# Performance work log

Measured on AMD Instinct MI355X. Metric: run time of the kernel, lower is better.

Reference implementation:

```python
import jax, jax.numpy as jnp
import numpy as np

N_USERS = 100000
N_ITEMS = 50000
N = N_USERS + N_ITEMS  # graph nodes
E = 2_400_000
B = 16384
EMB = 64
HID = 128
LN_EPS = 1e-5


def _gcn(x, W, b, src, dst):
    # PyG GCNConv (eval): sym-normalized aggregation with self-loops.
    xw = x @ W                                      # [N, out]
    deg = jnp.ones((N,), x.dtype).at[dst].add(1.0)  # in-degree + self-loop
    dinv = jax.lax.rsqrt(deg)
    norm = dinv[src] * dinv[dst]                    # [E]
    msg = xw[src] * norm[:, None]                   # [E, out] gather
    out = jax.ops.segment_sum(msg, dst, num_segments=N)
    out = out + xw * (dinv * dinv)[:, None]         # self-loop term (norm_ii = 1/deg_i)
    return out + b


def _ln(h, g, b):
    mu = jnp.mean(h, axis=-1, keepdims=True)
    var = jnp.mean(jnp.square(h - mu), axis=-1, keepdims=True)
    return (h - mu) * jax.lax.rsqrt(var + LN_EPS) * g + b


def setup_inputs() -> dict:
    key = jax.random.key(0)
    ks = jax.random.split(key, 20)
    f32 = jnp.float32
    def lin(k, fi, fo):
        return jax.random.normal(k, (fi, fo), f32) * (1.0 / np.sqrt(fi))
    inp = {
        "x": jax.random.normal(ks[0], (N, EMB), f32),
        "src": jax.random.randint(ks[1], (E,), 0, N, jnp.int32),
        "dst": jax.random.randint(ks[2], (E,), 0, N, jnp.int32),
        "user_indices": jax.random.randint(ks[3], (B,), 1, N_USERS + 1, jnp.int32),
        "item_indices": jax.random.randint(ks[4], (B,), 1, N_ITEMS + 1, jnp.int32),
        # GCNConv weights
        "W1": lin(ks[5], EMB, HID), "b1": jnp.zeros((HID,), f32),
        "W2": lin(ks[6], HID, EMB), "b2": jnp.zeros((EMB,), f32),
        # MLP head: Linear(128,128)-LN-ReLU-Linear(128,64)-LN-ReLU-Linear(64,1)
        "fcW1": lin(ks[7], 2 * EMB, HID), "fcb1": jnp.zeros((HID,), f32),
        "g1": jnp.ones((HID,), f32), "be1": jnp.zeros((HID,), f32),
        "fcW2": lin(ks[8], HID, HID // 2), "fcb2": jnp.zeros((HID // 2,), f32),
        "g2": jnp.ones((HID // 2,), f32), "be2": jnp.zeros((HID // 2,), f32),
        "fcW3": lin(ks[9], HID // 2, 1), "fcb3": jnp.zeros((1,), f32),
    }
    return inp


def reference(x, src, dst, user_indices, item_indices,
              W1, b1, W2, b2,
              fcW1, fcb1, g1, be1, fcW2, fcb2, g2, be2, fcW3, fcb3):
    # graph path (edge_index and x provided); dropout inactive in eval mode
    h = jax.nn.relu(_gcn(x, W1, b1, src, dst))
    h = _gcn(h, W2, b2, src, dst)                   # [N, EMB]
    user_emb = h[:N_USERS][user_indices - 1]        # [B, EMB]
    item_emb = h[N_USERS:][item_indices - 1]        # [B, EMB]
    c = jnp.concatenate([user_emb, item_emb], axis=1)  # [B, 2*EMB]
    z = jax.nn.relu(_ln(c @ fcW1 + fcb1, g1, be1))
    z = jax.nn.relu(_ln(z @ fcW2 + fcb2, g2, be2))
    z = z @ fcW3 + fcb3                             # [B, 1]
    return jax.nn.sigmoid(z).squeeze()
```

## Files before the change

### kernel.cpp

```cpp
#include <hip/hip_runtime.h>
#include <hip/hip_bf16.h>
#include <math.h>

#define N_USERS_C 100000
#define BK_SHIFT 9
#define BK_NODES 512
#define CPAD 16

typedef __bf16 bf8_t __attribute__((ext_vector_type(8)));
typedef float f32x4 __attribute__((ext_vector_type(4)));

__device__ __forceinline__ unsigned int pack_bf16(float a, float b) {
    __hip_bfloat16 ha = __float2bfloat16(a), hb = __float2bfloat16(b);
    return ((unsigned int)(*(unsigned short*)&hb) << 16) | (unsigned int)(*(unsigned short*)&ha);
}
__device__ __forceinline__ unsigned short bf16_1(float a) {
    __hip_bfloat16 ha = __float2bfloat16(a);
    return *(unsigned short*)&ha;
}
__device__ __forceinline__ float bf_lo(unsigned int u) { return __uint_as_float(u << 16); }
__device__ __forceinline__ float bf_hi(unsigned int u) { return __uint_as_float(u & 0xffff0000u); }

__global__ __launch_bounds__(512) void k_pre(const int* __restrict__ dst, int* __restrict__ chist,
                                             const float* __restrict__ x, unsigned int* __restrict__ xb,
                                             const float* __restrict__ W1, const float* __restrict__ W2,
                                             unsigned int* __restrict__ w1p, unsigned int* __restrict__ w2p,
                                             int E, int nbk, int EB2, int n2, int XB) {
    __shared__ int lcnt[BK_NODES];
    const int bid = blockIdx.x;
    const int t = threadIdx.x;
    if (bid < EB2) {
        if (t < nbk) lcnt[t] = 0;
        __syncthreads();
        int e0 = bid * 4096;
        #pragma unroll
        for (int j = 0; j < 8; ++j) {
            int e = e0 + j * 512 + t;
            if (e < E) atomicAdd(&lcnt[dst[e] >> BK_SHIFT], 1);
        }
        __syncthreads();
        if (t < nbk && lcnt[t]) atomicAdd(&chist[t * CPAD], lcnt[t]);
    } else if (bid < EB2 + XB) {
        int base = (bid - EB2) * 2048;
        #pragma unroll
        for (int j = 0; j < 4; ++j) {
            int i = base + j * 512 + t;
            if (i < n2) {
                float2 v = ((const float2*)x)[i];
                xb[i] = pack_bf16(v.x, v.y);
            }
        }
    } else if (bid == EB2 + XB) {
        #pragma unroll
        for (int j = 0; j < 8; ++j) {
            int i = j * 512 + t;
            int kp = i >> 7, n = i & 127;
            w1p[n * 32 + kp] = pack_bf16(W1[(size_t)(2 * kp) * 128 + n],
                                         W1[(size_t)(2 * kp + 1) * 128 + n]);
        }
    } else {
        #pragma unroll
        for (int j = 0; j < 8; ++j) {
            int i = j * 512 + t;
            int kp = i >> 6, n = i & 63;
            w2p[n * 64 + kp] = pack_bf16(W2[(size_t)(2 * kp) * 64 + n],
                                         W2[(size_t)(2 * kp + 1) * 64 + n]);
        }
    }
}

__global__ __launch_bounds__(512) void k_bin(const int* __restrict__ src,
                                             const int* __restrict__ dst,
                                             const int* __restrict__ chist,
                                             int* __restrict__ bcursor0,
                                             int* __restrict__ pairBuf, int E, int nbk) {
    __shared__ int lcnt[BK_NODES];
    __shared__ int lofs[BK_NODES];
    __shared__ int delta[BK_NODES];
    __shared__ int waveSum[8];
    __shared__ int sPack[4096];
    __shared__ unsigned short sBkt[4096];
    const int t = threadIdx.x;
    const int lane = t & 63;
    const int w = t >> 6;
    const int e0 = blockIdx.x * 4096;
    if (t < nbk) lcnt[t] = 0;
    __syncthreads();

    int mySrc[8], myB[8], myDl[8];
    #pragma unroll
    for (int j = 0; j < 8; ++j) {
        int e = e0 + j * 512 + t;
        if (e < E) {
            int sv = src[e], dv = dst[e];
            mySrc[j] = sv; myB[j] = dv >> BK_SHIFT; myDl[j] = dv & (BK_NODES - 1);
            atomicAdd(&lcnt[myB[j]], 1);
        } else myB[j] = -1;
    }
    __syncthreads();

    int v = (t < nbk) ? lcnt[t] : 0;
    int inc = v;
    #pragma unroll
    for (int off = 1; off < 64; off <<= 1) {
        int n = __shfl_up(inc, off);
        if (lane >= off) inc += n;
    }
    if (lane == 63) waveSum[w] = inc;
    int cv = (t < nbk) ? chist[t * CPAD] : 0;
    int cinc = cv;
    #pragma unroll
    for (int off = 1; off < 64; off <<= 1) {
        int n = __shfl_up(cinc, off);
        if (lane >= off) cinc += n;
    }
    __shared__ int cWaveSum[8];
    if (lane == 63) cWaveSum[w] = cinc;
    __syncthreads();
    int wp = 0, cwp = 0;
    #pragma unroll
    for (int i = 0; i < 8; ++i) {
        wp += (i < w) ? waveSum[i] : 0;
        cwp += (i < w) ? cWaveSum[i] : 0;
    }
    int ex = wp + inc - v;
    int cbase = cwp + cinc - cv;
    if (t < nbk) {
        lofs[t] = ex;
        int gb = cbase + ((v > 0) ? atomicAdd(&bcursor0[t * CPAD], v) : 0);
        delta[t] = gb - ex;
    }
    __syncthreads();

    #pragma unroll
    for (int j = 0; j < 8; ++j) {
        if (myB[j] >= 0) {
            int p = atomicAdd(&lofs[myB[j]], 1);
            sPack[p] = mySrc[j] | (myDl[j] << 18);
            sBkt[p] = (unsigned short)myB[j];
        }
    }
    __syncthreads();
    int total = (E - e0 < 4096) ? (E - e0) : 4096;
    for (int i = t; i < total; i += 512)
        pairBuf[delta[sBkt[i]] + i] = sPack[i];
}

__global__ __launch_bounds__(512) void k_bscatter(const int* __restrict__ pairBuf,
                                                  const int* __restrict__ chist,
                                                  int* __restrict__ rowstart,
                                                  float* __restrict__ dinv,
                                                  int* __restrict__ csr,
                                                  unsigned int* __restrict__ xb,
                                                  int N, int E, int nbk) {
    const int b = blockIdx.x;
    const int n0 = b << BK_SHIFT;
    int nn = N - n0; if (nn > BK_NODES) nn = BK_NODES;
    __shared__ int hist[BK_NODES];
    __shared__ int curs[BK_NODES];
    __shared__ float sdv[BK_NODES];
    __shared__ int waveSum[8];
    __shared__ int sE0, sE1;
    const int t = threadIdx.x;
    const int lane = t & 63;
    const int w = t >> 6;

    {
        int cv = (t < nbk) ? chist[t * CPAD] : 0;
        int cinc = cv;
        #pragma unroll
        for (int off = 1; off < 64; off <<= 1) {
            int n = __shfl_up(cinc, off);
            if (lane >= off) cinc += n;
        }
        if (lane == 63) waveSum[w] = cinc;
        if (t < nn) hist[t] = 0;
        __syncthreads();
        int cwp = 0;
        #pragma unroll
        for (int i = 0; i < 8; ++i) cwp += (i < w) ? waveSum[i] : 0;
        if (t == b) { sE0 = cwp + cinc - cv; sE1 = cwp + cinc; }
    }
    __syncthreads();
    const int e0 = sE0, e1 = sE1;

    {
        int e = e0 + t;
        for (; e + 1536 < e1; e += 2048) {
            int p0 = pairBuf[e], p1 = pairBuf[e + 512];
            int p2 = pairBuf[e + 1024], p3 = pairBuf[e + 1536];
            atomicAdd(&hist[p0 >> 18], 1);
            atomicAdd(&hist[p1 >> 18], 1);
            atomicAdd(&hist[p2 >> 18], 1);
            atomicAdd(&hist[p3 >> 18], 1);
        }
        for (; e < e1; e += 512)
            atomicAdd(&hist[pairBuf[e] >> 18], 1);
    }
    __syncthreads();

    int v = (t < nn) ? hist[t] : 0;
    int inc = v;
    #pragma unroll
    for (int off = 1; off < 64; off <<= 1) {
        int n = __shfl_up(inc, off);
        if (lane >= off) inc += n;
    }
    if (lane == 63) waveSum[w] = inc;
    __syncthreads();
    int wp = 0;
    #pragma unroll
    for (int i = 0; i < 8; ++i) wp += (i < w) ? waveSum[i] : 0;
    int ex = wp + inc - v;
    if (t < nn) {
        int r = e0 + ex;
        rowstart[n0 + t] = r;
        curs[t] = r;
        float dv = rsqrtf((float)(v + 1));
        dinv[n0 + t] = dv;
        sdv[t] = dv;
    }
    if (b == gridDim.x - 1 && t == 0) rowstart[N] = E;
    __syncthreads();
    {
        int e = e0 + t;
        for (; e + 1536 < e1; e += 2048) {
            int p0 = pairBuf[e], p1 = pairBuf[e + 512];
            int p2 = pairBuf[e + 1024], p3 = pairBuf[e + 1536];
            int q0 = atomicAdd(&curs[p0 >> 18], 1); csr[q0] = p0 & 0x3FFFF;
            int q1 = atomicAdd(&curs[p1 >> 18], 1); csr[q1] = p1 & 0x3FFFF;
            int q2 = atomicAdd(&curs[p2 >> 18], 1); csr[q2] = p2 & 0x3FFFF;
            int q3 = atomicAdd(&curs[p3 >> 18], 1); csr[q3] = p3 & 0x3FFFF;
        }
        for (; e < e1; e += 512) {
            int pk = pairBuf[e];
            int pos = atomicAdd(&curs[pk >> 18], 1);
            csr[pos] = pk & 0x3FFFF;
        }
    }
    {
        uint4* xb4 = (uint4*)(xb + (size_t)n0 * 32);
        int tot = nn * 8;
        for (int j = t; j < tot; j += 1024) {
            int j2 = j + 512;
            uint4 u = xb4[j];
            uint4 u2;
            bool two = (j2 < tot);
            if (two) u2 = xb4[j2];
            float dv = sdv[j >> 3];
            u.x = pack_bf16(dv * bf_lo(u.x), dv * bf_hi(u.x));
            u.y = pack_bf16(dv * bf_lo(u.y), dv * bf_hi(u.y));
            u.z = pack_bf16(dv * bf_lo(u.z), dv * bf_hi(u.z));
            u.w = pack_bf16(dv * bf_lo(u.w), dv * bf_hi(u.w));
            xb4[j] = u;
            if (two) {
                float dv2 = sdv[j2 >> 3];
                u2.x = pack_bf16(dv2 * bf_lo(u2.x), dv2 * bf_hi(u2.x));
                u2.y = pack_bf16(dv2 * bf_lo(u2.y), dv2 * bf_hi(u2.y));
                u2.z = pack_bf16(dv2 * bf_lo(u2.z), dv2 * bf_hi(u2.z));
                u2.w = pack_bf16(dv2 * bf_lo(u2.w), dv2 * bf_hi(u2.w));
                xb4[j2] = u2;
            }
        }
    }
}

__global__ __launch_bounds__(256) void k_gather1(const int* __restrict__ rowstart,
                                                 const int* __restrict__ csr,
                                                 const float* __restrict__ dinv,
                                                 const uint4* __restrict__ xb4,
                                                 unsigned int* __restrict__ outb, int N) {
    const int l = threadIdx.x & 63;
    const int w = threadIdx.x >> 6;
    const int half = l >> 5;
    const int h = l & 31;
    const int sub = h >> 3;
    const int c = h & 7;
    const int hb = half * 32;
    const int node = blockIdx.x * 8 + w * 2 + half;
    if (node >= N) return;
    const int rs = rowstart[node];
    const int re = rowstart[node + 1];
    uint4 us = xb4[(size_t)node * 8 + c];
    float dd = dinv[node];

    float acc[8] = {0.f, 0.f, 0.f, 0.f, 0.f, 0.f, 0.f, 0.f};
    for (int base = rs; base < re; base += 32) {
        int idx = base + h;
        int sE = (idx < re) ? csr[idx] : 0;
        int cnt = re - base; if (cnt > 32) cnt = 32;
        int groups = (cnt + 3) >> 2;
        uint4 u0, u1, u2, u3;
        {
            int sk;
            if (0 < groups) { sk = __shfl(sE, hb + 0 + sub);  u0 = xb4[(size_t)sk * 8 + c]; }
            if (1 < groups) { sk = __shfl(sE, hb + 4 + sub);  u1 = xb4[(size_t)sk * 8 + c]; }
            if (2 < groups) { sk = __shfl(sE, hb + 8 + sub);  u2 = xb4[(size_t)sk * 8 + c]; }
            if (3 < groups) { sk = __shfl(sE, hb + 12 + sub); u3 = xb4[(size_t)sk * 8 + c]; }
        }
        #define ACC8(uu) { acc[0] += bf_lo(uu.x); acc[1] += bf_hi(uu.x); \
                           acc[2] += bf_lo(uu.y); acc[3] += bf_hi(uu.y); \
                           acc[4] += bf_lo(uu.z); acc[5] += bf_hi(uu.z); \
                           acc[6] += bf_lo(uu.w); acc[7] += bf_hi(uu.w); }
        for (int g = 0; g < groups; g += 4) {
            uint4 c0 = u0, c1 = u1, c2 = u2, c3 = u3;
            {
                int sk;
                if (g + 4 < groups) { sk = __shfl(sE, hb + (g + 4) * 4 + sub); u0 = xb4[(size_t)sk * 8 + c]; }
                if (g + 5 < groups) { sk = __shfl(sE, hb + (g + 5) * 4 + sub); u1 = xb4[(size_t)sk * 8 + c]; }
                if (g + 6 < groups) { sk = __shfl(sE, hb + (g + 6) * 4 + sub); u2 = xb4[(size_t)sk * 8 + c]; }
                if (g + 7 < groups) { sk = __shfl(sE, hb + (g + 7) * 4 + sub); u3 = xb4[(size_t)sk * 8 + c]; }
            }
            if ((g + 0) * 4 + sub < cnt) ACC8(c0);
            if ((g + 1) * 4 + sub < cnt) ACC8(c1);
            if ((g + 2) * 4 + sub < cnt) ACC8(c2);
            if ((g + 3) * 4 + sub < cnt) ACC8(c3);
        }
    }
    #pragma unroll
    for (int m = 8; m < 32; m <<= 1)
        #pragma unroll
        for (int i = 0; i < 8; ++i) acc[i] += __shfl_xor(acc[i], m);
    if (sub == 0) {
        uint4 o;
        o.x = pack_bf16(dd * (acc[0] + bf_lo(us.x)), dd * (acc[1] + bf_hi(us.x)));
        o.y = pack_bf16(dd * (acc[2] + bf_lo(us.y)), dd * (acc[3] + bf_hi(us.y)));
        o.z = pack_bf16(dd * (acc[4] + bf_lo(us.z)), dd * (acc[5] + bf_hi(us.z)));
        o.w = pack_bf16(dd * (acc[6] + bf_lo(us.w)), dd * (acc[7] + bf_hi(us.w)));
        ((uint4*)outb)[(size_t)node * 8 + c] = o;
    }
}

__global__ __launch_bounds__(256) void k_layer12(const unsigned int* __restrict__ aggXb,
                                                 const unsigned int* __restrict__ w1p,
                                                 const float* __restrict__ b1,
                                                 const unsigned int* __restrict__ w2p,
                                                 const float* __restrict__ dinv,
                                                 unsigned int* __restrict__ xs2b, int N) {
    __shared__ unsigned int sA[64 * 36];
    __shared__ unsigned int sB[128 * 36];
    __shared__ unsigned int sC[64 * 68];
    const int t = threadIdx.x;
    const int w = t >> 6;
    const int l = t & 63;
    const int n16 = l & 15;
    const int quad = l >> 4;
    const int row0 = blockIdx.x * 64;

    for (int i = t; i < 512; i += 256) {
        int r = i >> 3, c = i & 7;
        int row = row0 + r;
        uint4 u = (row < N) ? ((const uint4*)aggXb)[(size_t)row * 8 + c]
                            : make_uint4(0u, 0u, 0u, 0u);
        *(uint4*)&sA[r * 36 + c * 4] = u;
    }
    {
        const uint4* w1p4 = (const uint4*)w1p;
        for (int j = t; j < 1024; j += 256) {
            int n = j >> 3, kp4 = j & 7;
            *(uint4*)&sB[n * 36 + kp4 * 4] = w1p4[j];
        }
    }
    __syncthreads();

    f32x4 acc[8];
    #pragma unroll
    for (int nt = 0; nt < 8; ++nt) acc[nt] = (f32x4){0.f, 0.f, 0.f, 0.f};
    {
        const int am = w * 16 + n16;
        bf8_t a0 = *(const bf8_t*)&sA[am * 36 + quad * 4];
        bf8_t a1 = *(const bf8_t*)&sA[am * 36 + 16 + quad * 4];
        #pragma unroll
        for (int nt = 0; nt < 8; ++nt) {
            bf8_t b0 = *(const bf8_t*)&sB[(nt * 16 + n16) * 36 + quad * 4];
            bf8_t b1v = *(const bf8_t*)&sB[(nt * 16 + n16) * 36 + 16 + quad * 4];
            acc[nt] = __builtin_amdgcn_mfma_f32_16x16x32_bf16(a0, b0, acc[nt], 0, 0, 0);
            acc[nt] = __builtin_amdgcn_mfma_f32_16x16x32_bf16(a1, b1v, acc[nt], 0, 0, 0);
        }
    }
    __syncthreads();

    {
        unsigned short* sC16 = (unsigned short*)sC;
        #pragma unroll
        for (int nt = 0; nt < 8; ++nt) {
            int col = nt * 16 + n16;
            float bv = b1[col];
            #pragma unroll
            for (int reg = 0; reg < 4; ++reg) {
                int r = w * 16 + quad * 4 + reg;
                sC16[r * 136 + col] = bf16_1(fmaxf(acc[nt][reg] + bv, 0.f));
            }
        }
    }
    {
        const uint4* w2p4 = (const uint4*)w2p;
        for (int j = t; j < 1024; j += 256) {
            int n = j >> 4, kp4 = j & 15;
            *(uint4*)&sB[n * 68 + kp4 * 4] = w2p4[j];
        }
    }
    __syncthreads();

    f32x4 acc2[4];
    #pragma unroll
    for (int nt = 0; nt < 4; ++nt) acc2[nt] = (f32x4){0.f, 0.f, 0.f, 0.f};
    {
        const int am = w * 16 + n16;
        #pragma unroll
        for (int ks = 0; ks < 4; ++ks) {
            bf8_t a = *(const bf8_t*)&sC[am * 68 + ks * 16 + quad * 4];
            #pragma unroll
            for (int nt = 0; nt < 4; ++nt) {
                bf8_t b = *(const bf8_t*)&sB[(nt * 16 + n16) * 68 + ks * 16 + quad * 4];
                acc2[nt] = __builtin_amdgcn_mfma_f32_16x16x32_bf16(a, b, acc2[nt], 0, 0, 0);
            }
        }
    }

    __syncthreads();
    {
        unsigned short* sA16 = (unsigned short*)sA;
        #pragma unroll
        for (int reg = 0; reg < 4; ++reg) {
            int r = w * 16 + quad * 4 + reg;
            int row = row0 + r;
            float dd = (row < N) ? dinv[row] : 0.f;
            #pragma unroll
            for (int nt = 0; nt < 4; ++nt)
                sA16[r * 72 + nt * 16 + n16] = bf16_1(acc2[nt][reg] * dd);
        }
    }
    __syncthreads();
    for (int i = t; i < 512; i += 256) {
        int r = i >> 3, c = i & 7;
        int row = row0 + r;
        if (row < N)
            ((uint4*)xs2b)[(size_t)row * 8 + c] = *(uint4*)&sA[r * 36 + c * 4];
    }
}

__global__ __launch_bounds__(256) void k_gather_pairs(const int* __restrict__ rowstart,
                                                      const int* __restrict__ csr,
                                                      const float* __restrict__ dinv,
                                                      const uint4* __restrict__ xs2b4,
                                                      const float* __restrict__ b2,
                                                      const int* __restrict__ ui,
                                                      const int* __restrict__ ii,
                                                      float* __restrict__ cB, int B) {
    const int w = threadIdx.x >> 6;
    const int b = blockIdx.x * 4 + w;
    const int l = threadIdx.x & 63;
    const int half = l >> 5;
    const int h = l & 31;
    const int sub = h >> 3;
    const int c = h & 7;
    const int hb = half * 32;
    if (b >= B) return;
    const int node = (half == 0) ? (ui[b] - 1) : (N_USERS_C + ii[b] - 1);
    const int rs = rowstart[node];
    const int re = rowstart[node + 1];
    uint4 us = xs2b4[(size_t)node * 8 + c];
    float dd = dinv[node];

    float acc[8] = {0.f, 0.f, 0.f, 0.f, 0.f, 0.f, 0.f, 0.f};
    for (int base = rs; base < re; base += 32) {
        int idx = base + h;
        int sE = (idx < re) ? csr[idx] : 0;
        int cnt = re - base; if (cnt > 32) cnt = 32;
        int groups = (cnt + 3) >> 2;
        uint4 u0, u1, u2, u3;
        {
            int sk;
            if (0 < groups) { sk = __shfl(sE, hb + 0 + sub);  u0 = xs2b4[(size_t)sk * 8 + c]; }
            if (1 < groups) { sk = __shfl(sE, hb + 4 + sub);  u1 = xs2b4[(size_t)sk * 8 + c]; }
            if (2 < groups) { sk = __shfl(sE, hb + 8 + sub);  u2 = xs2b4[(size_t)sk * 8 + c]; }
            if (3 < groups) { sk = __shfl(sE, hb + 12 + sub); u3 = xs2b4[(size_t)sk * 8 + c]; }
        }
        for (int g = 0; g < groups; g += 4) {
            uint4 c0 = u0, c1 = u1, c2 = u2, c3 = u3;
            {
                int sk;
                if (g + 4 < groups) { sk = __shfl(sE, hb + (g + 4) * 4 + sub); u0 = xs2b4[(size_t)sk * 8 + c]; }
                if (g + 5 < groups) { sk = __shfl(sE, hb + (g + 5) * 4 + sub); u1 = xs2b4[(size_t)sk * 8 + c]; }
                if (g + 6 < groups) { sk = __shfl(sE, hb + (g + 6) * 4 + sub); u2 = xs2b4[(size_t)sk * 8 + c]; }
                if (g + 7 < groups) { sk = __shfl(sE, hb + (g + 7) * 4 + sub); u3 = xs2b4[(size_t)sk * 8 + c]; }
            }
            if ((g + 0) * 4 + sub < cnt) ACC8(c0);
            if ((g + 1) * 4 + sub < cnt) ACC8(c1);
            if ((g + 2) * 4 + sub < cnt) ACC8(c2);
            if ((g + 3) * 4 + sub < cnt) ACC8(c3);
        }
    }
    #pragma unroll
    for (int m = 8; m < 32; m <<= 1)
        #pragma unroll
        for (int i = 0; i < 8; ++i) acc[i] += __shfl_xor(acc[i], m);
    if (sub == 0) {
        float4 s0, s1;
        s0.x = bf_lo(us.x); s0.y = bf_hi(us.x); s0.z = bf_lo(us.y); s0.w = bf_hi(us.y);
        s1.x = bf_lo(us.z); s1.y = bf_hi(us.z); s1.z = bf_lo(us.w); s1.w = bf_hi(us.w);
        float4 bb0 = ((const float4*)b2)[c * 2];
        float4 bb1 = ((const float4*)b2)[c * 2 + 1];
        float4 o0, o1;
        o0.x = dd * (acc[0] + s0.x) + bb0.x;
        o0.y = dd * (acc[1] + s0.y) + bb0.y;
        o0.z = dd * (acc[2] + s0.z) + bb0.z;
        o0.w = dd * (acc[3] + s0.w) + bb0.w;
        o1.x = dd * (acc[4] + s1.x) + bb1.x;
        o1.y = dd * (acc[5] + s1.y) + bb1.y;
        o1.z = dd * (acc[6] + s1.z) + bb1.z;
        o1.w = dd * (acc[7] + s1.w) + bb1.w;
        ((float4*)cB)[(size_t)b * 32 + half * 16 + c * 2] = o0;
        ((float4*)cB)[(size_t)b * 32 + half * 16 + c * 2 + 1] = o1;
    }
}

__global__ __launch_bounds__(256) void k_mlp(const float* __restrict__ cB,
                                             const float* __restrict__ fcW1, const float* __restrict__ fcb1,
                                             const float* __restrict__ g1,   const float* __restrict__ be1,
                                             const float* __restrict__ fcW2, const float* __restrict__ fcb2,
                                             const float* __restrict__ g2,   const float* __restrict__ be2,
                                             const float* __restrict__ fcW3, const float* __restrict__ fcb3,
                                             float* __restrict__ out) {
    __shared__ float sIn[32 * 128];
    __shared__ float sW[64 * 128];
    const int t = threadIdx.x;
    const int row0 = blockIdx.x * 32;
    const int rg = t >> 4;
    const int cg = t & 15;

    for (int i = t; i < 1024; i += 256) {
        int r = i >> 5, c4 = i & 31;
        *(float4*)&sIn[r * 128 + c4 * 4] = *(const float4*)&cB[(size_t)(row0 + r) * 128 + c4 * 4];
    }

    float acc1[2][8];
    {
        float4 b01 = *(const float4*)&fcb1[cg * 8];
        float4 b23 = *(const float4*)&fcb1[cg * 8 + 4];
        #pragma unroll
        for (int jj = 0; jj < 2; ++jj) {
            acc1[jj][0] = b01.x; acc1[jj][1] = b01.y; acc1[jj][2] = b01.z; acc1[jj][3] = b01.w;
            acc1[jj][4] = b23.x; acc1[jj][5] = b23.y; acc1[jj][6] = b23.z; acc1[jj][7] = b23.w;
        }
    }
    for (int s = 0; s < 2; ++s) {
        __syncthreads();
        for (int i = t; i < 2048; i += 256) {
            int k = i >> 5, c4 = i & 31;
            *(float4*)&sW[k * 128 + c4 * 4] = *(const float4*)&fcW1[(size_t)(64 * s + k) * 128 + c4 * 4];
        }
        __syncthreads();
        for (int k0 = 0; k0 < 64; k0 += 4) {
            float4 a[2];
            #pragma unroll
            for (int jj = 0; jj < 2; ++jj)
                a[jj] = *(const float4*)&sIn[(rg * 2 + jj) * 128 + 64 * s + k0];
            #pragma unroll
            for (int kk = 0; kk < 4; ++kk) {
                float4 w0 = *(const float4*)&sW[(k0 + kk) * 128 + cg * 8];
                float4 w1 = *(const float4*)&sW[(k0 + kk) * 128 + cg * 8 + 4];
                #pragma unroll
                for (int jj = 0; jj < 2; ++jj) {
                    float f = ((const float*)&a[jj])[kk];
                    acc1[jj][0] += f * w0.x; acc1[jj][1] += f * w0.y;
                    acc1[jj][2] += f * w0.z; acc1[jj][3] += f * w0.w;
                    acc1[jj][4] += f * w1.x; acc1[jj][5] += f * w1.y;
                    acc1[jj][6] += f * w1.z; acc1[jj][7] += f * w1.w;
                }
            }
        }
    }
    __syncthreads();

    {
        float4 g01 = *(const float4*)&g1[cg * 8];
        float4 g23 = *(const float4*)&g1[cg * 8 + 4];
        float4 e01 = *(const float4*)&be1[cg * 8];
        float4 e23 = *(const float4*)&be1[cg * 8 + 4];
        float gv[8] = {g01.x, g01.y, g01.z, g01.w, g23.x, g23.y, g23.z, g23.w};
        float ev[8] = {e01.x, e01.y, e01.z, e01.w, e23.x, e23.y, e23.z, e23.w};
        #pragma unroll
        for (int jj = 0; jj < 2; ++jj) {
            float s_ = 0.f, ss = 0.f;
            #pragma unroll
            for (int c = 0; c < 8; ++c) { float v = acc1[jj][c]; s_ += v; ss += v * v; }
            #pragma unroll
            for (int m = 1; m < 16; m <<= 1) { s_ += __shfl_xor(s_, m); ss += __shfl_xor(ss, m); }
            float mu = s_ * (1.0f / 128.0f);
            float var = ss * (1.0f / 128.0f) - mu * mu;
            float rs = rsqrtf(var + 1e-5f);
            #pragma unroll
            for (int c = 0; c < 8; ++c) {
                float z = (acc1[jj][c] - mu) * rs * gv[c] + ev[c];
                sIn[(rg * 2 + jj) * 128 + cg * 8 + c] = fmaxf(z, 0.f);
            }
        }
    }
    __syncthreads();

    for (int i = t; i < 2048; i += 256) {
        int k = i >> 4, c4 = i & 15;
        *(float4*)&sW[k * 64 + c4 * 4] = *(const float4*)&fcW2[(size_t)k * 64 + c4 * 4];
    }
    float acc2[2][4];
    {
        float4 bv = *(const float4*)&fcb2[cg * 4];
        #pragma unroll
        for (int jj = 0; jj < 2; ++jj) {
            acc2[jj][0] = bv.x; acc2[jj][1] = bv.y; acc2[jj][2] = bv.z; acc2[jj][3] = bv.w;
        }
    }
    __syncthreads();
    for (int k0 = 0; k0 < 128; k0 += 4) {
        float4 a[2], w[4];
        #pragma unroll
        for (int jj = 0; jj < 2; ++jj) a[jj] = *(const float4*)&sIn[(rg * 2 + jj) * 128 + k0];
        #pragma unroll
        for (int kk = 0; kk < 4; ++kk) w[kk] = *(const float4*)&sW[(k0 + kk) * 64 + cg * 4];
        #pragma unroll
        for (int jj = 0; jj < 2; ++jj) {
            const float* aj = (const float*)&a[jj];
            #pragma unroll
            for (int kk = 0; kk < 4; ++kk) {
                float f = aj[kk];
                acc2[jj][0] += f * w[kk].x; acc2[jj][1] += f * w[kk].y;
                acc2[jj][2] += f * w[kk].z; acc2[jj][3] += f * w[kk].w;
            }
        }
    }

    {
        float4 gv4 = *(const float4*)&g2[cg * 4];
        float4 ev4 = *(const float4*)&be2[cg * 4];
        float4 w34 = *(const float4*)&fcW3[cg * 4];
        float gv[4] = {gv4.x, gv4.y, gv4.z, gv4.w};
        float ev[4] = {ev4.x, ev4.y, ev4.z, ev4.w};
        float wv[4] = {w34.x, w34.y, w34.z, w34.w};
        float b3 = fcb3[0];
        #pragma unroll
        for (int jj = 0; jj < 2; ++jj) {
            float s_ = 0.f, ss = 0.f;
            #pragma unroll
            for (int c = 0; c < 4; ++c) { float v = acc2[jj][c]; s_ += v; ss += v * v; }
            #pragma unroll
            for (int m = 1; m < 16; m <<= 1) { s_ += __shfl_xor(s_, m); ss += __shfl_xor(ss, m); }
            float mu = s_ * (1.0f / 64.0f);
            float var = ss * (1.0f / 64.0f) - mu * mu;
            float rs = rsqrtf(var + 1e-5f);
            float p = 0.f;
            #pragma unroll
            for (int c = 0; c < 4; ++c) {
                float z = fmaxf((acc2[jj][c] - mu) * rs * gv[c] + ev[c], 0.f);
                p += z * wv[c];
            }
            #pragma unroll
            for (int m = 1; m < 16; m <<= 1) p += __shfl_xor(p, m);
            if (cg == 0) out[row0 + rg * 2 + jj] = 1.0f / (1.0f + expf(-(p + b3)));
        }
    }
}

extern "C" void kernel_launch(void* const* d_in, const int* in_sizes, int n_in,
                              void* d_out, int out_size, void* d_ws, size_t ws_size,
                              hipStream_t stream) {
    const float* x    = (const float*)d_in[0];
    const int*   src  = (const int*)d_in[1];
    const int*   dst  = (const int*)d_in[2];
    const int*   ui   = (const int*)d_in[3];
    const int*   ii   = (const int*)d_in[4];
    const float* W1   = (const float*)d_in[5];
    const float* b1   = (const float*)d_in[6];
    const float* W2   = (const float*)d_in[7];
    const float* b2   = (const float*)d_in[8];
    const float* fcW1 = (const float*)d_in[9];
    const float* fcb1 = (const float*)d_in[10];
    const float* g1   = (const float*)d_in[11];
    const float* be1  = (const float*)d_in[12];
    const float* fcW2 = (const float*)d_in[13];
    const float* fcb2 = (const float*)d_in[14];
    const float* g2   = (const float*)d_in[15];
    const float* be2  = (const float*)d_in[16];
    const float* fcW3 = (const float*)d_in[17];
    const float* fcb3 = (const float*)d_in[18];
    float* out = (float*)d_out;

    const int N = in_sizes[0] / 64;
    const int E = in_sizes[1];
    const int B = in_sizes[3];
    const int NBK = (N + BK_NODES - 1) >> BK_SHIFT;
    const int EB2 = (E + 4095) / 4096;
    const int n2 = N * 32;
    const int XB = (n2 + 2047) / 2048;

    float* ws   = (float*)d_ws;
    float* dinv = ws;
    int* rowstart = (int*)(dinv + N);
    int* csr      = rowstart + (N + 1);
    unsigned int* xb = (unsigned int*)(csr + E);
    unsigned int* bufU = xb + (size_t)N * 32;
    unsigned int* xs2b = bufU + (size_t)N * 32;
    float* cB = (float*)(xs2b + (size_t)N * 32);
    unsigned int* w1p = (unsigned int*)(cB + (size_t)B * 128);
    unsigned int* w2p = w1p + 4096;
    int* pairBuf = (int*)bufU;
    int* chist   = pairBuf + E;
    int* bcursor = chist + 512 * CPAD;
    unsigned int* aggXb = bufU;

    hipMemsetAsync(chist, 0, 2 * 512 * CPAD * sizeof(int), stream);
    k_pre<<<EB2 + XB + 2, 512, 0, stream>>>(dst, chist, x, xb, W1, W2, w1p, w2p,
                                            E, NBK, EB2, n2, XB);
    k_bin<<<EB2, 512, 0, stream>>>(src, dst, chist, bcursor, pairBuf, E, NBK);
    k_bscatter<<<NBK, 512, 0, stream>>>(pairBuf, chist, rowstart, dinv, csr, xb, N, E, NBK);

    k_gather1<<<(N + 7) / 8, 256, 0, stream>>>(rowstart, csr, dinv, (const uint4*)xb, aggXb, N);

    k_layer12<<<(N + 63) / 64, 256, 0, stream>>>(aggXb, w1p, b1, w2p, dinv, xs2b, N);

    k_gather_pairs<<<(B + 3) / 4, 256, 0, stream>>>(rowstart, csr, dinv, (const uint4*)xs2b,
                                                    b2, ui, ii, cB, B);

    k_mlp<<<B / 32, 256, 0, stream>>>(cB, fcW1, fcb1, g1, be1,
                                      fcW2, fcb2, g2, be2, fcW3, fcb3, out);
}
```

Baseline: 331.6 us.

## Compute per-node degree histogram early and move degree scaling into binning kernel

k_pre now builds a per-node in-degree histogram with global atomics while it counts destination buckets. k_bscatter therefore no longer makes a separate pass over pairBuf with shared-memory atomics to count degrees. The dinv computation and the bf16 x pre-scaling move from k_bscatter, which has few blocks, into the tail of k_bin, which has more blocks. This removes one full read pass over the edge pairs and lightens the low-parallelism scatter kernel, at the cost of 2.4M random global atomics and a larger memset.

Result: slower. 419.2 us (+26.4%).

```diff
diff --git a/kernel.cpp b/kernel.cpp
--- a/kernel.cpp
+++ b/kernel.cpp
@@ -22,6 +22,7 @@
 __device__ __forceinline__ float bf_hi(unsigned int u) { return __uint_as_float(u & 0xffff0000u); }
 
 __global__ __launch_bounds__(512) void k_pre(const int* __restrict__ dst, int* __restrict__ chist,
+                                             int* __restrict__ nhist,
                                              const float* __restrict__ x, unsigned int* __restrict__ xb,
                                              const float* __restrict__ W1, const float* __restrict__ W2,
                                              unsigned int* __restrict__ w1p, unsigned int* __restrict__ w2p,
@@ -36,7 +37,11 @@
         #pragma unroll
         for (int j = 0; j < 8; ++j) {
             int e = e0 + j * 512 + t;
-            if (e < E) atomicAdd(&lcnt[dst[e] >> BK_SHIFT], 1);
+            if (e < E) {
+                int dv = dst[e];
+                atomicAdd(&lcnt[dv >> BK_SHIFT], 1);
+                atomicAdd(&nhist[dv], 1);
+            }
         }
         __syncthreads();
         if (t < nbk && lcnt[t]) atomicAdd(&chist[t * CPAD], lcnt[t]);
@@ -73,7 +78,11 @@
                                              const int* __restrict__ dst,
                                              const int* __restrict__ chist,
                                              int* __restrict__ bcursor0,
-                                             int* __restrict__ pairBuf, int E, int nbk) {
+                                             int* __restrict__ pairBuf,
+                                             const int* __restrict__ nhist,
+                                             float* __restrict__ dinv,
+                                             unsigned int* __restrict__ xb,
+                                             int E, int nbk, int N) {
     __shared__ int lcnt[BK_NODES];
     __shared__ int lofs[BK_NODES];
     __shared__ int delta[BK_NODES];
@@ -144,21 +153,50 @@
     int total = (E - e0 < 4096) ? (E - e0) : 4096;
     for (int i = t; i < total; i += 512)
         pairBuf[delta[sBkt[i]] + i] = sPack[i];
+
+    {
+        uint4* xb4 = (uint4*)xb;
+        const int nbase = blockIdx.x * 256;
+        const int c4 = t & 7;
+        const int na = nbase + (t >> 3);
+        int n1 = na, n2_ = na + 64, n3 = na + 128, n4 = na + 192;
+        bool v1 = n1 < N, v2 = n2_ < N, v3 = n3 < N, v4 = n4 < N;
+        int h1_ = 0, h2_ = 0, h3_ = 0, h4_ = 0;
+        if (v1) h1_ = nhist[n1];
+        if (v2) h2_ = nhist[n2_];
+        if (v3) h3_ = nhist[n3];
+        if (v4) h4_ = nhist[n4];
+        uint4 u1, u2, u3, u4;
+        if (v1) u1 = xb4[(size_t)n1 * 8 + c4];
+        if (v2) u2 = xb4[(size_t)n2_ * 8 + c4];
+        if (v3) u3 = xb4[(size_t)n3 * 8 + c4];
+        if (v4) u4 = xb4[(size_t)n4 * 8 + c4];
+        #define SCALE_ST(vv, nn, uu, hh)  if (vv) { \
+            float dv_ = rsqrtf((float)(hh + 1)); \
+            uu.x = pack_bf16(dv_ * bf_lo(uu.x), dv_ * bf_hi(uu.x)); \
+            uu.y = pack_bf16(dv_ * bf_lo(uu.y), dv_ * bf_hi(uu.y)); \
+            uu.z = pack_bf16(dv_ * bf_lo(uu.z), dv_ * bf_hi(uu.z)); \
+            uu.w = pack_bf16(dv_ * bf_lo(uu.w), dv_ * bf_hi(uu.w)); \
+            xb4[(size_t)nn * 8 + c4] = uu; \
+            if (c4 == 0) dinv[nn] = dv_; }
+        SCALE_ST(v1, n1, u1, h1_);
+        SCALE_ST(v2, n2_, u2, h2_);
+        SCALE_ST(v3, n3, u3, h3_);
+        SCALE_ST(v4, n4, u4, h4_);
+        #undef SCALE_ST
+    }
 }
 
 __global__ __launch_bounds__(512) void k_bscatter(const int* __restrict__ pairBuf,
                                                   const int* __restrict__ chist,
+                                                  const int* __restrict__ nhist,
                                                   int* __restrict__ rowstart,
-                                                  float* __restrict__ dinv,
                                                   int* __restrict__ csr,
-                                                  unsigned int* __restrict__ xb,
                                                   int N, int E, int nbk) {
     const int b = blockIdx.x;
     const int n0 = b << BK_SHIFT;
     int nn = N - n0; if (nn > BK_NODES) nn = BK_NODES;
-    __shared__ int hist[BK_NODES];
     __shared__ int curs[BK_NODES];
-    __shared__ float sdv[BK_NODES];
     __shared__ int waveSum[8];
     __shared__ int sE0, sE1;
     const int t = threadIdx.x;
@@ -174,7 +212,6 @@
             if (lane >= off) cinc += n;
         }
         if (lane == 63) waveSum[w] = cinc;
-        if (t < nn) hist[t] = 0;
         __syncthreads();
         int cwp = 0;
         #pragma unroll
@@ -184,22 +221,7 @@
     __syncthreads();
     const int e0 = sE0, e1 = sE1;
 
-    {
-        int e = e0 + t;
-        for (; e + 1536 < e1; e += 2048) {
-            int p0 = pairBuf[e], p1 = pairBuf[e + 512];
-            int p2 = pairBuf[e + 1024], p3 = pairBuf[e + 1536];
-            atomicAdd(&hist[p0 >> 18], 1);
-            atomicAdd(&hist[p1 >> 18], 1);
-            atomicAdd(&hist[p2 >> 18], 1);
-            atomicAdd(&hist[p3 >> 18], 1);
-        }
-        for (; e < e1; e += 512)
-            atomicAdd(&hist[pairBuf[e] >> 18], 1);
-    }
-    __syncthreads();
-
-    int v = (t < nn) ? hist[t] : 0;
+    int v = (t < nn) ? nhist[n0 + t] : 0;
     int inc = v;
     #pragma unroll
     for (int off = 1; off < 64; off <<= 1) {
@@ -216,9 +238,6 @@
         int r = e0 + ex;
         rowstart[n0 + t] = r;
         curs[t] = r;
-        float dv = rsqrtf((float)(v + 1));
-        dinv[n0 + t] = dv;
-        sdv[t] = dv;
     }
     if (b == gridDim.x - 1 && t == 0) rowstart[N] = E;
     __syncthreads();
@@ -236,31 +255,6 @@
             int pk = pairBuf[e];
             int pos = atomicAdd(&curs[pk >> 18], 1);
             csr[pos] = pk & 0x3FFFF;
-        }
-    }
-    {
-        uint4* xb4 = (uint4*)(xb + (size_t)n0 * 32);
-        int tot = nn * 8;
-        for (int j = t; j < tot; j += 1024) {
-            int j2 = j + 512;
-            uint4 u = xb4[j];
-            uint4 u2;
-            bool two = (j2 < tot);
-            if (two) u2 = xb4[j2];
-            float dv = sdv[j >> 3];
-            u.x = pack_bf16(dv * bf_lo(u.x), dv * bf_hi(u.x));
-            u.y = pack_bf16(dv * bf_lo(u.y), dv * bf_hi(u.y));
-            u.z = pack_bf16(dv * bf_lo(u.z), dv * bf_hi(u.z));
-            u.w = pack_bf16(dv * bf_lo(u.w), dv * bf_hi(u.w));
-            xb4[j] = u;
-            if (two) {
-                float dv2 = sdv[j2 >> 3];
-                u2.x = pack_bf16(dv2 * bf_lo(u2.x), dv2 * bf_hi(u2.x));
-                u2.y = pack_bf16(dv2 * bf_lo(u2.y), dv2 * bf_hi(u2.y));
-                u2.z = pack_bf16(dv2 * bf_lo(u2.z), dv2 * bf_hi(u2.z));
-                u2.w = pack_bf16(dv2 * bf_lo(u2.w), dv2 * bf_hi(u2.w));
-                xb4[j2] = u2;
-            }
         }
     }
 }
@@ -707,13 +701,15 @@
     int* pairBuf = (int*)bufU;
     int* chist   = pairBuf + E;
     int* bcursor = chist + 512 * CPAD;
+    int* nhist   = bcursor + 512 * CPAD;
     unsigned int* aggXb = bufU;
 
-    hipMemsetAsync(chist, 0, 2 * 512 * CPAD * sizeof(int), stream);
-    k_pre<<<EB2 + XB + 2, 512, 0, stream>>>(dst, chist, x, xb, W1, W2, w1p, w2p,
+    hipMemsetAsync(chist, 0, (size_t)(2 * 512 * CPAD + N) * sizeof(int), stream);
+    k_pre<<<EB2 + XB + 2, 512, 0, stream>>>(dst, chist, nhist, x, xb, W1, W2, w1p, w2p,
                                             E, NBK, EB2, n2, XB);
-    k_bin<<<EB2, 512, 0, stream>>>(src, dst, chist, bcursor, pairBuf, E, NBK);
-    k_bscatter<<<NBK, 512, 0, stream>>>(pairBuf, chist, rowstart, dinv, csr, xb, N, E, NBK);
+    k_bin<<<EB2, 512, 0, stream>>>(src, dst, chist, bcursor, pairBuf,
+                                   nhist, dinv, xb, E, NBK, N);
+    k_bscatter<<<NBK, 512, 0, stream>>>(pairBuf, chist, nhist, rowstart, csr, N, E, NBK);
 
     k_gather1<<<(N + 7) / 8, 256, 0, stream>>>(rowstart, csr, dinv, (const uint4*)xb, aggXb, N);
 
```

## Fuse layer-1 neighbor gather into the two-layer MFMA GEMM kernel

Applied to the files above, without the earlier changes.

Merges the first-layer sparse aggregation kernel into the dense layer-1/layer-2 GEMM kernel. Each 512-thread block gathers neighbor features for its 64 rows straight into shared memory, so the intermediate aggregated buffer no longer makes a global round trip and one launch is removed. The MFMA work is split across 8 waves by row and column, and occupancy is hinted at 6 blocks per SM via launch bounds. The gather phase now sits in the same block as the GEMM, so load imbalance from skewed degrees can stall the whole block, and the GEMM phase cannot overlap with other blocks' gathers the way separate kernels allowed.

After: 331.1 us. No clear change (-0.2%).

```diff
diff --git a/kernel.cpp b/kernel.cpp
--- a/kernel.cpp
+++ b/kernel.cpp
@@ -20,6 +20,11 @@
 }
 __device__ __forceinline__ float bf_lo(unsigned int u) { return __uint_as_float(u << 16); }
 __device__ __forceinline__ float bf_hi(unsigned int u) { return __uint_as_float(u & 0xffff0000u); }
+
+#define ACC8(uu) { acc[0] += bf_lo(uu.x); acc[1] += bf_hi(uu.x); \
+                   acc[2] += bf_lo(uu.y); acc[3] += bf_hi(uu.y); \
+                   acc[4] += bf_lo(uu.z); acc[5] += bf_hi(uu.z); \
+                   acc[6] += bf_lo(uu.w); acc[7] += bf_hi(uu.w); }
 
 __global__ __launch_bounds__(512) void k_pre(const int* __restrict__ dst, int* __restrict__ chist,
                                              const float* __restrict__ x, unsigned int* __restrict__ xb,
@@ -265,117 +270,112 @@
     }
 }
 
-__global__ __launch_bounds__(256) void k_gather1(const int* __restrict__ rowstart,
+__global__ __launch_bounds__(512, 6) void k_gl12(const int* __restrict__ rowstart,
                                                  const int* __restrict__ csr,
                                                  const float* __restrict__ dinv,
                                                  const uint4* __restrict__ xb4,
-                                                 unsigned int* __restrict__ outb, int N) {
-    const int l = threadIdx.x & 63;
-    const int w = threadIdx.x >> 6;
-    const int half = l >> 5;
-    const int h = l & 31;
-    const int sub = h >> 3;
-    const int c = h & 7;
-    const int hb = half * 32;
-    const int node = blockIdx.x * 8 + w * 2 + half;
-    if (node >= N) return;
-    const int rs = rowstart[node];
-    const int re = rowstart[node + 1];
-    uint4 us = xb4[(size_t)node * 8 + c];
-    float dd = dinv[node];
-
-    float acc[8] = {0.f, 0.f, 0.f, 0.f, 0.f, 0.f, 0.f, 0.f};
-    for (int base = rs; base < re; base += 32) {
-        int idx = base + h;
-        int sE = (idx < re) ? csr[idx] : 0;
-        int cnt = re - base; if (cnt > 32) cnt = 32;
-        int groups = (cnt + 3) >> 2;
-        uint4 u0, u1, u2, u3;
-        {
-            int sk;
-            if (0 < groups) { sk = __shfl(sE, hb + 0 + sub);  u0 = xb4[(size_t)sk * 8 + c]; }
-            if (1 < groups) { sk = __shfl(sE, hb + 4 + sub);  u1 = xb4[(size_t)sk * 8 + c]; }
-            if (2 < groups) { sk = __shfl(sE, hb + 8 + sub);  u2 = xb4[(size_t)sk * 8 + c]; }
-            if (3 < groups) { sk = __shfl(sE, hb + 12 + sub); u3 = xb4[(size_t)sk * 8 + c]; }
-        }
-        #define ACC8(uu) { acc[0] += bf_lo(uu.x); acc[1] += bf_hi(uu.x); \
-                           acc[2] += bf_lo(uu.y); acc[3] += bf_hi(uu.y); \
-                           acc[4] += bf_lo(uu.z); acc[5] += bf_hi(uu.z); \
-                           acc[6] += bf_lo(uu.w); acc[7] += bf_hi(uu.w); }
-        for (int g = 0; g < groups; g += 4) {
-            uint4 c0 = u0, c1 = u1, c2 = u2, c3 = u3;
-            {
-                int sk;
-                if (g + 4 < groups) { sk = __shfl(sE, hb + (g + 4) * 4 + sub); u0 = xb4[(size_t)sk * 8 + c]; }
-                if (g + 5 < groups) { sk = __shfl(sE, hb + (g + 5) * 4 + sub); u1 = xb4[(size_t)sk * 8 + c]; }
-                if (g + 6 < groups) { sk = __shfl(sE, hb + (g + 6) * 4 + sub); u2 = xb4[(size_t)sk * 8 + c]; }
-                if (g + 7 < groups) { sk = __shfl(sE, hb + (g + 7) * 4 + sub); u3 = xb4[(size_t)sk * 8 + c]; }
-            }
-            if ((g + 0) * 4 + sub < cnt) ACC8(c0);
-            if ((g + 1) * 4 + sub < cnt) ACC8(c1);
-            if ((g + 2) * 4 + sub < cnt) ACC8(c2);
-            if ((g + 3) * 4 + sub < cnt) ACC8(c3);
-        }
-    }
-    #pragma unroll
-    for (int m = 8; m < 32; m <<= 1)
-        #pragma unroll
-        for (int i = 0; i < 8; ++i) acc[i] += __shfl_xor(acc[i], m);
-    if (sub == 0) {
-        uint4 o;
-        o.x = pack_bf16(dd * (acc[0] + bf_lo(us.x)), dd * (acc[1] + bf_hi(us.x)));
-        o.y = pack_bf16(dd * (acc[2] + bf_lo(us.y)), dd * (acc[3] + bf_hi(us.y)));
-        o.z = pack_bf16(dd * (acc[4] + bf_lo(us.z)), dd * (acc[5] + bf_hi(us.z)));
-        o.w = pack_bf16(dd * (acc[6] + bf_lo(us.w)), dd * (acc[7] + bf_hi(us.w)));
-        ((uint4*)outb)[(size_t)node * 8 + c] = o;
-    }
-}
-
-__global__ __launch_bounds__(256) void k_layer12(const unsigned int* __restrict__ aggXb,
                                                  const unsigned int* __restrict__ w1p,
                                                  const float* __restrict__ b1,
                                                  const unsigned int* __restrict__ w2p,
-                                                 const float* __restrict__ dinv,
                                                  unsigned int* __restrict__ xs2b, int N) {
     __shared__ unsigned int sA[64 * 36];
     __shared__ unsigned int sB[128 * 36];
     __shared__ unsigned int sC[64 * 68];
     const int t = threadIdx.x;
     const int w = t >> 6;
+    const int wr = w & 3;
+    const int wn = w >> 2;
     const int l = t & 63;
+    const int half = l >> 5;
+    const int h = l & 31;
+    const int sub = h >> 3;
+    const int c = h & 7;
+    const int hb = half * 32;
     const int n16 = l & 15;
     const int quad = l >> 4;
     const int row0 = blockIdx.x * 64;
 
-    for (int i = t; i < 512; i += 256) {
-        int r = i >> 3, c = i & 7;
-        int row = row0 + r;
-        uint4 u = (row < N) ? ((const uint4*)aggXb)[(size_t)row * 8 + c]
-                            : make_uint4(0u, 0u, 0u, 0u);
-        *(uint4*)&sA[r * 36 + c * 4] = u;
-    }
     {
         const uint4* w1p4 = (const uint4*)w1p;
-        for (int j = t; j < 1024; j += 256) {
+        for (int j = t; j < 1024; j += 512) {
             int n = j >> 3, kp4 = j & 7;
             *(uint4*)&sB[n * 36 + kp4 * 4] = w1p4[j];
         }
     }
-    __syncthreads();
-
-    f32x4 acc[8];
-    #pragma unroll
-    for (int nt = 0; nt < 8; ++nt) acc[nt] = (f32x4){0.f, 0.f, 0.f, 0.f};
-    {
-        const int am = w * 16 + n16;
+
+    for (int it = 0; it < 4; ++it) {
+        const int r = w * 8 + it * 2 + half;
+        const int node = row0 + r;
+        float acc[8] = {0.f, 0.f, 0.f, 0.f, 0.f, 0.f, 0.f, 0.f};
+        uint4 us = make_uint4(0u, 0u, 0u, 0u);
+        float dd = 0.f;
+        if (node < N) {
+            const int rs = rowstart[node];
+            const int re = rowstart[node + 1];
+            us = xb4[(size_t)node * 8 + c];
+            dd = dinv[node];
+            for (int base = rs; base < re; base += 32) {
+                int idx = base + h;
+                int sE = (idx < re) ? csr[idx] : 0;
+                int cnt = re - base; if (cnt > 32) cnt = 32;
+                int groups = (cnt + 3) >> 2;
+                uint4 u0, u1, u2, u3;
+                {
+                    int sk;
+                    if (0 < groups) { sk = __shfl(sE, hb + 0 + sub);  u0 = xb4[(size_t)sk * 8 + c]; }
+                    if (1 < groups) { sk = __shfl(sE, hb + 4 + sub);  u1 = xb4[(size_t)sk * 8 + c]; }
+                    if (2 < groups) { sk = __shfl(sE, hb + 8 + sub);  u2 = xb4[(size_t)sk * 8 + c]; }
+                    if (3 < groups) { sk = __shfl(sE, hb + 12 + sub); u3 = xb4[(size_t)sk * 8 + c]; }
+                }
+                for (int g = 0; g < groups; g += 4) {
+                    uint4 c0 = u0, c1 = u1, c2 = u2, c3 = u3;
+                    {
+                        int sk;
+                        if (g + 4 < groups) { sk = __shfl(sE, hb + (g + 4) * 4 + sub); u0 = xb4[(size_t)sk * 8 + c]; }
+                        if (g + 5 < groups) { sk = __shfl(sE, hb + (g + 5) * 4 + sub); u1 = xb4[(size_t)sk * 8 + c]; }
+                        if (g + 6 < groups) { sk = __shfl(sE, hb + (g + 6) * 4 + sub); u2 = xb4[(size_t)sk * 8 + c]; }
+                        if (g + 7 < groups) { sk = __shfl(sE, hb + (g + 7) * 4 + sub); u3 = xb4[(size_t)sk * 8 + c]; }
+                    }
+                    if ((g + 0) * 4 + sub < cnt) ACC8(c0);
+                    if ((g + 1) * 4 + sub < cnt) ACC8(c1);
+                    if ((g + 2) * 4 + sub < cnt) ACC8(c2);
+                    if ((g + 3) * 4 + sub < cnt) ACC8(c3);
+                }
+            }
+        }
+        #pragma unroll
+        for (int m = 8; m < 32; m <<= 1)
+            #pragma unroll
+            for (int i = 0; i < 8; ++i) acc[i] += __shfl_xor(acc[i], m);
+        if (sub == 0) {
+            uint4 o;
+            if (node < N) {
+                o.x = pack_bf16(dd * (acc[0] + bf_lo(us.x)), dd * (acc[1] + bf_hi(us.x)));
+                o.y = pack_bf16(dd * (acc[2] + bf_lo(us.y)), dd * (acc[3] + bf_hi(us.y)));
+                o.z = pack_bf16(dd * (acc[4] + bf_lo(us.z)), dd * (acc[5] + bf_hi(us.z)));
+                o.w = pack_bf16(dd * (acc[6] + bf_lo(us.w)), dd * (acc[7] + bf_hi(us.w)));
+            } else {
+                o = make_uint4(0u, 0u, 0u, 0u);
+            }
+            *(uint4*)&sA[r * 36 + c * 4] = o;
+        }
+    }
+    __syncthreads();
+
+    f32x4 acc1[4];
+    #pragma unroll
+    for (int k = 0; k < 4; ++k) acc1[k] = (f32x4){0.f, 0.f, 0.f, 0.f};
+    {
+        const int am = wr * 16 + n16;
         bf8_t a0 = *(const bf8_t*)&sA[am * 36 + quad * 4];
         bf8_t a1 = *(const bf8_t*)&sA[am * 36 + 16 + quad * 4];
         #pragma unroll
-        for (int nt = 0; nt < 8; ++nt) {
+        for (int k = 0; k < 4; ++k) {
+            int nt = wn * 4 + k;
             bf8_t b0 = *(const bf8_t*)&sB[(nt * 16 + n16) * 36 + quad * 4];
             bf8_t b1v = *(const bf8_t*)&sB[(nt * 16 + n16) * 36 + 16 + quad * 4];
-            acc[nt] = __builtin_amdgcn_mfma_f32_16x16x32_bf16(a0, b0, acc[nt], 0, 0, 0);
-            acc[nt] = __builtin_amdgcn_mfma_f32_16x16x32_bf16(a1, b1v, acc[nt], 0, 0, 0);
+            acc1[k] = __builtin_amdgcn_mfma_f32_16x16x32_bf16(a0, b0, acc1[k], 0, 0, 0);
+            acc1[k] = __builtin_amdgcn_mfma_f32_16x16x32_bf16(a1, b1v, acc1[k], 0, 0, 0);
         }
     }
     __syncthreads();
@@ -383,60 +383,64 @@
     {
         unsigned short* sC16 = (unsigned short*)sC;
         #pragma unroll
-        for (int nt = 0; nt < 8; ++nt) {
-            int col = nt * 16 + n16;
+        for (int k = 0; k < 4; ++k) {
+            int col = (wn * 4 + k) * 16 + n16;
             float bv = b1[col];
             #pragma unroll
             for (int reg = 0; reg < 4; ++reg) {
-                int r = w * 16 + quad * 4 + reg;
-                sC16[r * 136 + col] = bf16_1(fmaxf(acc[nt][reg] + bv, 0.f));
+                int r = wr * 16 + quad * 4 + reg;
+                sC16[r * 136 + col] = bf16_1(fmaxf(acc1[k][reg] + bv, 0.f));
             }
         }
     }
     {
         const uint4* w2p4 = (const uint4*)w2p;
-        for (int j = t; j < 1024; j += 256) {
+        for (int j = t; j < 1024; j += 512) {
             int n = j >> 4, kp4 = j & 15;
             *(uint4*)&sB[n * 68 + kp4 * 4] = w2p4[j];
         }
     }
     __syncthreads();
 
-    f32x4 acc2[4];
-    #pragma unroll
-    for (int nt = 0; nt < 4; ++nt) acc2[nt] = (f32x4){0.f, 0.f, 0.f, 0.f};
-    {
-        const int am = w * 16 + n16;
+    f32x4 acc2[2];
+    #pragma unroll
+    for (int k = 0; k < 2; ++k) acc2[k] = (f32x4){0.f, 0.f, 0.f, 0.f};
+    {
+        const int am = wr * 16 + n16;
         #pragma unroll
         for (int ks = 0; ks < 4; ++ks) {
             bf8_t a = *(const bf8_t*)&sC[am * 68 + ks * 16 + quad * 4];
             #pragma unroll
-            for (int nt = 0; nt < 4; ++nt) {
+            for (int k = 0; k < 2; ++k) {
+                int nt = wn * 2 + k;
                 bf8_t b = *(const bf8_t*)&sB[(nt * 16 + n16) * 68 + ks * 16 + quad * 4];
-                acc2[nt] = __builtin_amdgcn_mfma_f32_16x16x32_bf16(a, b, acc2[nt], 0, 0, 0);
-            }
-        }
-    }
-
-    __syncthreads();
+                acc2[k] = __builtin_amdgcn_mfma_f32_16x16x32_bf16(a, b, acc2[k], 0, 0, 0);
+            }
+        }
+    }
+    __syncthreads();
+
     {
         unsigned short* sA16 = (unsigned short*)sA;
         #pragma unroll
         for (int reg = 0; reg < 4; ++reg) {
-            int r = w * 16 + quad * 4 + reg;
+            int r = wr * 16 + quad * 4 + reg;
             int row = row0 + r;
-            float dd = (row < N) ? dinv[row] : 0.f;
-            #pragma unroll
-            for (int nt = 0; nt < 4; ++nt)
-                sA16[r * 72 + nt * 16 + n16] = bf16_1(acc2[nt][reg] * dd);
-        }
-    }
-    __syncthreads();
-    for (int i = t; i < 512; i += 256) {
-        int r = i >> 3, c = i & 7;
+            float dd2 = (row < N) ? dinv[row] : 0.f;
+            #pragma unroll
+            for (int k = 0; k < 2; ++k) {
+                int nt = wn * 2 + k;
+                sA16[r * 72 + nt * 16 + n16] = bf16_1(acc2[k][reg] * dd2);
+            }
+        }
+    }
+    __syncthreads();
+    {
+        int i = t;
+        int r = i >> 3, cc = i & 7;
         int row = row0 + r;
         if (row < N)
-            ((uint4*)xs2b)[(size_t)row * 8 + c] = *(uint4*)&sA[r * 36 + c * 4];
+            ((uint4*)xs2b)[(size_t)row * 8 + cc] = *(uint4*)&sA[r * 36 + cc * 4];
     }
 }
 
@@ -707,7 +711,6 @@
     int* pairBuf = (int*)bufU;
     int* chist   = pairBuf + E;
     int* bcursor = chist + 512 * CPAD;
-    unsigned int* aggXb = bufU;
 
     hipMemsetAsync(chist, 0, 2 * 512 * CPAD * sizeof(int), stream);
     k_pre<<<EB2 + XB + 2, 512, 0, stream>>>(dst, chist, x, xb, W1, W2, w1p, w2p,
@@ -715,9 +718,8 @@
     k_bin<<<EB2, 512, 0, stream>>>(src, dst, chist, bcursor, pairBuf, E, NBK);
     k_bscatter<<<NBK, 512, 0, stream>>>(pairBuf, chist, rowstart, dinv, csr, xb, N, E, NBK);
 
-    k_gather1<<<(N + 7) / 8, 256, 0, stream>>>(rowstart, csr, dinv, (const uint4*)xb, aggXb, N);
-
-    k_layer12<<<(N + 63) / 64, 256, 0, stream>>>(aggXb, w1p, b1, w2p, dinv, xs2b, N);
+    k_gl12<<<(N + 63) / 64, 512, 0, stream>>>(rowstart, csr, dinv, (const uint4*)xb,
+                                              w1p, b1, w2p, xs2b, N);
 
     k_gather_pairs<<<(B + 3) / 4, 256, 0, stream>>>(rowstart, csr, dinv, (const uint4*)xs2b,
                                                     b2, ui, ii, cB, B);
```
